# Optimization experiments

Measured on AMD Instinct MI355X. Metric: run time of the kernel, lower is better.

The kernel has to match this reference:

```python
import jax, jax.numpy as jnp
import numpy as np

E = 8        # num_experts
K = 2        # top_k
CAP = 512    # hard-coded capacity in MoELayer
H = 2048     # hidden_dim
F = 8192     # ffn_dim


def setup_inputs() -> dict:
    key = jax.random.key(0)
    ks = jax.random.split(key, 6)
    inp = {
        "hidden_states": jax.random.normal(ks[0], (2, 1024, H), jnp.float32),
        "router_w": jax.random.normal(ks[1], (E, H), jnp.float32) * (0.01 / np.sqrt(H)),
        "w1": jax.random.normal(ks[2], (F, H), jnp.float32) * (1.0 / np.sqrt(H)),
        "b1": jax.random.normal(ks[3], (F,), jnp.float32) * 0.01,
        "w2": jax.random.normal(ks[4], (H, F), jnp.float32) * (1.0 / np.sqrt(F)),
        "b2": jax.random.normal(ks[5], (H,), jnp.float32) * 0.01,
    }
    return inp


def reference(hidden_states, router_w, w1, b1, w2, b2):
    orig_shape = hidden_states.shape
    x = hidden_states.reshape(-1, H)          # [N, H]
    N = x.shape[0]

    # --- Router: softmax then top-k ---
    logits = x @ router_w.T                   # [N, E]
    probs = jax.nn.softmax(logits, axis=-1)
    top_p, top_i = jax.lax.top_k(probs, K)    # [N, K]

    # --- Capacity-based permute (slot-major order: all slot-0 tokens, then slot-1,
    # matching the torch loop over top_k slots within each expert) ---
    expert_flat = top_i.T.reshape(-1)         # [K*N] int
    probs_flat = top_p.T.reshape(-1)          # [K*N]
    token_idx = jnp.tile(jnp.arange(N), K)    # [K*N]

    onehot = (expert_flat[:, None] == jnp.arange(E)[None, :]).astype(jnp.int32)  # [K*N, E]
    # position of each routed token within its expert's queue
    pos = jnp.take_along_axis(jnp.cumsum(onehot, axis=0), expert_flat[:, None], axis=1)[:, 0] - 1
    keep = pos < CAP                          # deterministic truncation at capacity
    dest = expert_flat * CAP + pos            # slot in [E*CAP] dispatch buffer
    dest_m = jnp.where(keep, dest, E * CAP)   # out-of-range -> dropped by scatter

    buf = jnp.zeros((E * CAP, H), x.dtype).at[dest_m].set(x[token_idx], mode='drop')

    # --- Shared expert FFN (all2all is identity on one device) ---
    h = jax.nn.gelu(buf @ w1.T + b1, approximate=False) @ w2.T + b2  # [E*CAP, H]

    # --- Weighted combine (scatter-add back to token positions) ---
    gathered = jnp.where(keep[:, None], h[jnp.where(keep, dest, 0)], 0.0) * probs_flat[:, None]
    out = jnp.zeros_like(x).at[token_idx].add(gathered)
    return out.reshape(orig_shape)
```

## Files before the change

### kernel.cpp

```cpp
#include <hip/hip_runtime.h>

#define HD 2048
#define FD 8192
#define NE 8
#define CAP 512

typedef __attribute__((ext_vector_type(4))) float f32x4;
typedef __attribute__((ext_vector_type(8))) __bf16 bf16x8;

__device__ __forceinline__ void gload_lds16(const __bf16* g, __bf16* l) {
    __builtin_amdgcn_global_load_lds(
        (const __attribute__((address_space(1))) void*)g,
        (__attribute__((address_space(3))) void*)l, 16, 0, 0);
}
__device__ __forceinline__ void waitv4() { asm volatile("s_waitcnt vmcnt(4)" ::: "memory"); }
__device__ __forceinline__ void waitv0() { asm volatile("s_waitcnt vmcnt(0)" ::: "memory"); }

__global__ __launch_bounds__(256) void cvt_k(const float* __restrict__ src,
                                             __bf16* __restrict__ dst, int n8) {
    int i = blockIdx.x * 256 + threadIdx.x;
    if (i >= n8) return;
    const float* s = src + (size_t)i * 8;
    f32x4 a = *(const f32x4*)s;
    f32x4 b = *(const f32x4*)(s + 4);
    bf16x8 o;
    o[0] = (__bf16)a[0]; o[1] = (__bf16)a[1]; o[2] = (__bf16)a[2]; o[3] = (__bf16)a[3];
    o[4] = (__bf16)b[0]; o[5] = (__bf16)b[1]; o[6] = (__bf16)b[2]; o[7] = (__bf16)b[3];
    *(bf16x8*)(dst + (size_t)i * 8) = o;
}

__global__ __launch_bounds__(256) void router_k(const float* __restrict__ x,
                                                const float* __restrict__ rw,
                                                int2* __restrict__ experts,
                                                float2* __restrict__ probs, int Ntok) {
    int wave = threadIdx.x >> 6, lane = threadIdx.x & 63;
    int n = blockIdx.x * 4 + wave;
    if (n >= Ntok) return;
    const float* xr = x + (size_t)n * HD;
    double acc[NE];
#pragma unroll
    for (int e = 0; e < NE; e++) acc[e] = 0.0;
    for (int i = 0; i < HD / 64; i++) {
        float xv = xr[lane + 64 * i];
#pragma unroll
        for (int e = 0; e < NE; e++)
            acc[e] += (double)xv * (double)rw[e * HD + lane + 64 * i];
    }
#pragma unroll
    for (int e = 0; e < NE; e++) {
        double v = acc[e];
        for (int off = 32; off > 0; off >>= 1) v += __shfl_xor(v, off);
        acc[e] = v;
    }
    if (lane == 0) {
        double mx = acc[0];
#pragma unroll
        for (int e = 1; e < NE; e++) mx = acc[e] > mx ? acc[e] : mx;
        double s = 0.0;
#pragma unroll
        for (int e = 0; e < NE; e++) s += exp(acc[e] - mx);
        float pf[NE];
#pragma unroll
        for (int e = 0; e < NE; e++) pf[e] = (float)(exp(acc[e] - mx) / s);
        int e0 = 0; float b0 = pf[0];
#pragma unroll
        for (int e = 1; e < NE; e++) if (pf[e] > b0) { b0 = pf[e]; e0 = e; }
        int e1 = -1; float b1 = -1.0f;
#pragma unroll
        for (int e = 0; e < NE; e++) if (e != e0 && pf[e] > b1) { b1 = pf[e]; e1 = e; }
        experts[n] = make_int2(e0, e1);
        probs[n] = make_float2(b0, b1);
    }
}

__global__ __launch_bounds__(256) void scan_k(const int2* __restrict__ experts,
                                              int* __restrict__ dest,
                                              int* __restrict__ slot_token, int Ntok) {
    __shared__ int cnts[256][NE];
    int tid = threadIdx.x;
    for (int i = tid; i < NE * CAP; i += 256) slot_token[i] = -1;
    int per = (2 * Ntok) / 256;
    int base = tid * per;
    int c[NE];
#pragma unroll
    for (int e = 0; e < NE; e++) c[e] = 0;
    int eloc[16];
    for (int i = 0; i < per; i++) {
        int j = base + i;
        int t = j & (Ntok - 1);
        int2 ex = experts[t];
        int e = (j >= Ntok) ? ex.y : ex.x;
        eloc[i] = e;
        c[e]++;
    }
#pragma unroll
    for (int e = 0; e < NE; e++) cnts[tid][e] = c[e];
    __syncthreads();
    if (tid < NE) {
        int run = 0;
        for (int t2 = 0; t2 < 256; t2++) { int v = cnts[t2][tid]; cnts[t2][tid] = run; run += v; }
    }
    __syncthreads();
    int b[NE];
#pragma unroll
    for (int e = 0; e < NE; e++) b[e] = cnts[tid][e];
    for (int i = 0; i < per; i++) {
        int j = base + i;
        int t = j & (Ntok - 1);
        int e = eloc[i];
        int pos = b[e]++;
        if (pos < CAP) {
            int d = e * CAP + pos;
            dest[j] = d;
            slot_token[d] = t;
        } else {
            dest[j] = -1;
        }
    }
}

__global__ __launch_bounds__(256) void dispatch_k(const float* __restrict__ x,
                                                  const int* __restrict__ slot_token,
                                                  __bf16* __restrict__ buf) {
    int slot = blockIdx.x;
    int tok = slot_token[slot];
    int idx = threadIdx.x * 8;
    __bf16* drow = buf + (size_t)slot * HD + idx;
    if (tok >= 0) {
        const float* srow = x + (size_t)tok * HD + idx;
        f32x4 a = *(const f32x4*)srow;
        f32x4 b = *(const f32x4*)(srow + 4);
        bf16x8 o;
        o[0] = (__bf16)a[0]; o[1] = (__bf16)a[1]; o[2] = (__bf16)a[2]; o[3] = (__bf16)a[3];
        o[4] = (__bf16)b[0]; o[5] = (__bf16)b[1]; o[6] = (__bf16)b[2]; o[7] = (__bf16)b[3];
        *(bf16x8*)drow = o;
    } else {
        f32x4 z = 0;
        *(f32x4*)drow = z;
    }
}

__device__ inline float gelu_exact(float v) {
    return 0.5f * v * (1.0f + erff(v * 0.70710678118654752f));
}

template <int EPI, int BM, int ALOADS, int QM>
__global__ __launch_bounds__(512) void gemm8p(const __bf16* __restrict__ A,
                                              const __bf16* __restrict__ B,
                                              const float* __restrict__ bias,
                                              void* __restrict__ Cout,
                                              int N, int K) {
    constexpr int MREP = 4 * QM;
    __shared__ __align__(16) __bf16 As[2][BM * 64];
    __shared__ __align__(16) __bf16 Bs[2][256 * 64];
    int m0 = blockIdx.y * BM, n0 = blockIdx.x * 256;
    int tid = threadIdx.x;
    int lane = tid & 63, wave = tid >> 6;
    int wr = wave >> 2, wc = wave & 3;
    int lrow = lane & 15, l16 = lane >> 4;
    int NT = K >> 6;

    int sr = tid >> 3;
    int c8 = tid & 7;
    int csw = (c8 ^ (sr & 7)) * 8;
    const __bf16* Ag = A + (size_t)(m0 + sr) * K + csw;
    const __bf16* Bg = B + (size_t)(n0 + sr) * K + csw;
    int ldst = sr * 64 + c8 * 8;

    int rch0 = ((0 + l16) ^ (lrow & 7)) * 8;
    int rch1 = ((4 + l16) ^ (lrow & 7)) * 8;

    f32x4 acc[MREP][4];
#pragma unroll
    for (int m = 0; m < MREP; m++)
#pragma unroll
        for (int n = 0; n < 4; n++) acc[m][n] = 0;

#pragma unroll
    for (int i = 0; i < ALOADS; i++)
        gload_lds16(Ag + (size_t)(i * 64) * K, &As[0][ldst + i * 4096]);
#pragma unroll
    for (int i = 0; i < 4; i++)
        gload_lds16(Bg + (size_t)(i * 64) * K, &Bs[0][ldst + i * 4096]);
#pragma unroll
    for (int i = 0; i < 4; i++)
        gload_lds16(Bg + (size_t)(i * 64) * K + 64, &Bs[1][ldst + i * 4096]);
    waitv4();
    __builtin_amdgcn_s_barrier();

    for (int t = 0; t < NT; ++t) {
        int p = t & 1;
        const __bf16* Asl = As[p];
        const __bf16* Bsl = Bs[p];
        bf16x8 bf[4][2];
#pragma unroll
        for (int q = 0; q < 4; ++q) {
            bf16x8 af[QM][2];
#pragma unroll
            for (int j = 0; j < QM; j++) {
                int row = (wr * (BM / 2) + (q * QM + j) * 16 + lrow) * 64;
                af[j][0] = *(const bf16x8*)&Asl[row + rch0];
                af[j][1] = *(const bf16x8*)&Asl[row + rch1];
            }
            if (q == 0) {
#pragma unroll
                for (int n = 0; n < 4; n++) {
                    int row = (wc * 64 + n * 16 + lrow) * 64;
                    bf[n][0] = *(const bf16x8*)&Bsl[row + rch0];
                    bf[n][1] = *(const bf16x8*)&Bsl[row + rch1];
                }
                if (t + 1 < NT) {
                    gload_lds16(Ag + (size_t)(t + 1) * 64, &As[(t + 1) & 1][ldst]);
                    gload_lds16(Ag + (size_t)64 * K + (size_t)(t + 1) * 64,
                                &As[(t + 1) & 1][ldst + 4096]);
                }
            } else if (q == 1) {
                if (ALOADS == 4 && t + 1 < NT) {
                    gload_lds16(Ag + (size_t)128 * K + (size_t)(t + 1) * 64,
                                &As[(t + 1) & 1][ldst + 8192]);
                    gload_lds16(Ag + (size_t)192 * K + (size_t)(t + 1) * 64,
                                &As[(t + 1) & 1][ldst + 12288]);
                }
            } else if (q == 2) {
                if (t + 2 < NT) {
                    gload_lds16(Bg + (size_t)(t + 2) * 64, &Bs[t & 1][ldst]);
                    gload_lds16(Bg + (size_t)64 * K + (size_t)(t + 2) * 64,
                                &Bs[t & 1][ldst + 4096]);
                }
            } else {
                if (t + 2 < NT) {
                    gload_lds16(Bg + (size_t)128 * K + (size_t)(t + 2) * 64,
                                &Bs[t & 1][ldst + 8192]);
                    gload_lds16(Bg + (size_t)192 * K + (size_t)(t + 2) * 64,
                                &Bs[t & 1][ldst + 12288]);
                }
            }
            __builtin_amdgcn_s_barrier();
            __builtin_amdgcn_s_setprio(1);
#pragma unroll
            for (int j = 0; j < QM; j++)
#pragma unroll
                for (int n = 0; n < 4; n++)
#pragma unroll
                    for (int kk = 0; kk < 2; kk++)
                        acc[q * QM + j][n] = __builtin_amdgcn_mfma_f32_16x16x32_bf16(
                            af[j][kk], bf[n][kk], acc[q * QM + j][n], 0, 0, 0);
            __builtin_amdgcn_s_setprio(0);
            if (q == 3) {
                if (t + 2 < NT) waitv4(); else waitv0();
            }
            __builtin_amdgcn_s_barrier();
        }
    }

    int col_base = n0 + wc * 64;
    int row_base0 = m0 + wr * (BM / 2) + l16 * 4;
#pragma unroll
    for (int n = 0; n < 4; n++) {
        int col = col_base + n * 16 + lrow;
        float bv = bias[col];
#pragma unroll
        for (int mf = 0; mf < MREP; mf++) {
            int row0 = row_base0 + mf * 16;
#pragma unroll
            for (int r = 0; r < 4; r++) {
                float v = acc[mf][n][r] + bv;
                if (EPI == 0) {
                    ((__bf16*)Cout)[(size_t)(row0 + r) * N + col] = (__bf16)gelu_exact(v);
                } else {
                    ((float*)Cout)[(size_t)(row0 + r) * N + col] = v;
                }
            }
        }
    }
}

__global__ __launch_bounds__(256) void combine_k(const float* __restrict__ h2,
                                                 const int* __restrict__ dest,
                                                 const float2* __restrict__ probs,
                                                 float* __restrict__ out, int Ntok) {
    int t = blockIdx.x;
    int d0 = dest[t], d1 = dest[Ntok + t];
    float2 p = probs[t];
    int idx = threadIdx.x * 8;
    f32x4 o0 = 0, o1 = 0;
    if (d0 >= 0) {
        const float* r = h2 + (size_t)d0 * HD + idx;
        o0 += p.x * (*(const f32x4*)r);
        o1 += p.x * (*(const f32x4*)(r + 4));
    }
    if (d1 >= 0) {
        const float* r = h2 + (size_t)d1 * HD + idx;
        o0 += p.y * (*(const f32x4*)r);
        o1 += p.y * (*(const f32x4*)(r + 4));
    }
    float* w = out + (size_t)t * HD + idx;
    *(f32x4*)w = o0;
    *(f32x4*)(w + 4) = o1;
}

extern "C" void kernel_launch(void* const* d_in, const int* in_sizes, int n_in,
                              void* d_out, int out_size, void* d_ws, size_t ws_size,
                              hipStream_t stream) {
    const float* x  = (const float*)d_in[0];
    const float* rw = (const float*)d_in[1];
    const float* w1 = (const float*)d_in[2];
    const float* b1 = (const float*)d_in[3];
    const float* w2 = (const float*)d_in[4];
    const float* b2 = (const float*)d_in[5];
    float* out = (float*)d_out;
    int Ntok = in_sizes[0] / HD;

    char* ws = (char*)d_ws;
    __bf16* w1b = (__bf16*)ws;            ws += (size_t)FD * HD * 2;
    __bf16* w2b = (__bf16*)ws;            ws += (size_t)HD * FD * 2;
    __bf16* buf = (__bf16*)ws;            ws += (size_t)NE * CAP * HD * 2;
    __bf16* h1  = (__bf16*)ws;            ws += (size_t)NE * CAP * FD * 2;
    float*  h2  = (float*)ws;             ws += (size_t)NE * CAP * HD * 4;
    int2*   experts = (int2*)ws;          ws += (size_t)Ntok * 8;
    float2* probsb  = (float2*)ws;        ws += (size_t)Ntok * 8;
    int*    dest    = (int*)ws;           ws += (size_t)2 * Ntok * 4;
    int*    slot_token = (int*)ws;        ws += (size_t)NE * CAP * 4;

    int n8 = FD * HD / 8;
    cvt_k<<<n8 / 256, 256, 0, stream>>>(w1, w1b, n8);
    cvt_k<<<n8 / 256, 256, 0, stream>>>(w2, w2b, n8);
    router_k<<<Ntok / 4, 256, 0, stream>>>(x, rw, experts, probsb, Ntok);
    scan_k<<<1, 256, 0, stream>>>(experts, dest, slot_token, Ntok);
    dispatch_k<<<NE * CAP, 256, 0, stream>>>(x, slot_token, buf);
    gemm8p<0, 256, 4, 2><<<dim3(FD / 256, (NE * CAP) / 256), 512, 0, stream>>>(
        buf, w1b, b1, (void*)h1, FD, HD);
    gemm8p<1, 128, 2, 1><<<dim3(HD / 256, (NE * CAP) / 128), 512, 0, stream>>>(
        h1, w2b, b2, (void*)h2, HD, FD);
    combine_k<<<Ntok, 256, 0, stream>>>(h2, dest, probsb, out, Ntok);
}
```

Baseline: 526.7 us.

## Software-pipeline A-fragment LDS reads across MFMA phases in gemm8p

Restructures the GEMM inner loop so each phase works on two 16-row A fragments. The next phase's A fragment is double-buffered in registers and loaded from LDS before the current phase's MFMAs, with a sched_barrier keeping the order. For the BM=128 GEMM this also changes the phase split from 4 phases of 1 fragment to 2 phases of 2, and regroups the B prefetch loads. The aim is to hide LDS read latency behind MFMA work and cut per-phase barrier overhead, at the cost of more VGPRs for the extra fragment buffers.

After: 563.9 us. 7.1% more time.

```diff
diff --git a/kernel.cpp b/kernel.cpp
--- a/kernel.cpp
+++ b/kernel.cpp
@@ -144,13 +144,15 @@
     return 0.5f * v * (1.0f + erff(v * 0.70710678118654752f));
 }
 
-template <int EPI, int BM, int ALOADS, int QM>
+template <int EPI, int BM>
 __global__ __launch_bounds__(512) void gemm8p(const __bf16* __restrict__ A,
                                               const __bf16* __restrict__ B,
                                               const float* __restrict__ bias,
                                               void* __restrict__ Cout,
                                               int N, int K) {
-    constexpr int MREP = 4 * QM;
+    constexpr int MREP = BM / 32;
+    constexpr int P = MREP / 2;
+    constexpr int ALOADS = BM / 64;
     __shared__ __align__(16) __bf16 As[2][BM * 64];
     __shared__ __align__(16) __bf16 Bs[2][256 * 64];
     int m0 = blockIdx.y * BM, n0 = blockIdx.x * 256;
@@ -189,64 +191,72 @@
     __builtin_amdgcn_s_barrier();
 
     for (int t = 0; t < NT; ++t) {
-        int p = t & 1;
-        const __bf16* Asl = As[p];
-        const __bf16* Bsl = Bs[p];
+        const __bf16* Asl = As[t & 1];
+        const __bf16* Bsl = Bs[t & 1];
+        __bf16* Anx = As[(t + 1) & 1];
+        __bf16* Bnx = Bs[t & 1];
         bf16x8 bf[4][2];
-#pragma unroll
-        for (int q = 0; q < 4; ++q) {
-            bf16x8 af[QM][2];
-#pragma unroll
-            for (int j = 0; j < QM; j++) {
-                int row = (wr * (BM / 2) + (q * QM + j) * 16 + lrow) * 64;
-                af[j][0] = *(const bf16x8*)&Asl[row + rch0];
-                af[j][1] = *(const bf16x8*)&Asl[row + rch1];
-            }
-            if (q == 0) {
-#pragma unroll
-                for (int n = 0; n < 4; n++) {
-                    int row = (wc * 64 + n * 16 + lrow) * 64;
-                    bf[n][0] = *(const bf16x8*)&Bsl[row + rch0];
-                    bf[n][1] = *(const bf16x8*)&Bsl[row + rch1];
-                }
-                if (t + 1 < NT) {
-                    gload_lds16(Ag + (size_t)(t + 1) * 64, &As[(t + 1) & 1][ldst]);
-                    gload_lds16(Ag + (size_t)64 * K + (size_t)(t + 1) * 64,
-                                &As[(t + 1) & 1][ldst + 4096]);
-                }
-            } else if (q == 1) {
-                if (ALOADS == 4 && t + 1 < NT) {
-                    gload_lds16(Ag + (size_t)128 * K + (size_t)(t + 1) * 64,
-                                &As[(t + 1) & 1][ldst + 8192]);
-                    gload_lds16(Ag + (size_t)192 * K + (size_t)(t + 1) * 64,
-                                &As[(t + 1) & 1][ldst + 12288]);
-                }
-            } else if (q == 2) {
-                if (t + 2 < NT) {
-                    gload_lds16(Bg + (size_t)(t + 2) * 64, &Bs[t & 1][ldst]);
-                    gload_lds16(Bg + (size_t)64 * K + (size_t)(t + 2) * 64,
-                                &Bs[t & 1][ldst + 4096]);
+        bf16x8 af[2][2][2];
+#pragma unroll
+        for (int n = 0; n < 4; n++) {
+            int row = (wc * 64 + n * 16 + lrow) * 64;
+            bf[n][0] = *(const bf16x8*)&Bsl[row + rch0];
+            bf[n][1] = *(const bf16x8*)&Bsl[row + rch1];
+        }
+#pragma unroll
+        for (int j = 0; j < 2; j++) {
+            int row = (wr * (BM / 2) + j * 16 + lrow) * 64;
+            af[0][j][0] = *(const bf16x8*)&Asl[row + rch0];
+            af[0][j][1] = *(const bf16x8*)&Asl[row + rch1];
+        }
+#pragma unroll
+        for (int q = 0; q < P; ++q) {
+            if (P == 4) {
+                if (q == 0 && t + 1 < NT) {
+                    gload_lds16(Ag + (size_t)(t + 1) * 64, Anx + ldst);
+                    gload_lds16(Ag + (size_t)64 * K + (size_t)(t + 1) * 64, Anx + ldst + 4096);
+                } else if (q == 1 && t + 1 < NT) {
+                    gload_lds16(Ag + (size_t)128 * K + (size_t)(t + 1) * 64, Anx + ldst + 8192);
+                    gload_lds16(Ag + (size_t)192 * K + (size_t)(t + 1) * 64, Anx + ldst + 12288);
+                } else if (q == 2 && t + 2 < NT) {
+                    gload_lds16(Bg + (size_t)(t + 2) * 64, Bnx + ldst);
+                    gload_lds16(Bg + (size_t)64 * K + (size_t)(t + 2) * 64, Bnx + ldst + 4096);
+                } else if (q == 3 && t + 2 < NT) {
+                    gload_lds16(Bg + (size_t)128 * K + (size_t)(t + 2) * 64, Bnx + ldst + 8192);
+                    gload_lds16(Bg + (size_t)192 * K + (size_t)(t + 2) * 64, Bnx + ldst + 12288);
                 }
             } else {
-                if (t + 2 < NT) {
-                    gload_lds16(Bg + (size_t)128 * K + (size_t)(t + 2) * 64,
-                                &Bs[t & 1][ldst + 8192]);
-                    gload_lds16(Bg + (size_t)192 * K + (size_t)(t + 2) * 64,
-                                &Bs[t & 1][ldst + 12288]);
+                if (q == 0 && t + 1 < NT) {
+                    gload_lds16(Ag + (size_t)(t + 1) * 64, Anx + ldst);
+                    gload_lds16(Ag + (size_t)64 * K + (size_t)(t + 1) * 64, Anx + ldst + 4096);
+                } else if (q == 1 && t + 2 < NT) {
+                    gload_lds16(Bg + (size_t)(t + 2) * 64, Bnx + ldst);
+                    gload_lds16(Bg + (size_t)64 * K + (size_t)(t + 2) * 64, Bnx + ldst + 4096);
+                    gload_lds16(Bg + (size_t)128 * K + (size_t)(t + 2) * 64, Bnx + ldst + 8192);
+                    gload_lds16(Bg + (size_t)192 * K + (size_t)(t + 2) * 64, Bnx + ldst + 12288);
                 }
             }
             __builtin_amdgcn_s_barrier();
+            if (q < P - 1) {
+#pragma unroll
+                for (int j = 0; j < 2; j++) {
+                    int row = (wr * (BM / 2) + ((q + 1) * 2 + j) * 16 + lrow) * 64;
+                    af[(q + 1) & 1][j][0] = *(const bf16x8*)&Asl[row + rch0];
+                    af[(q + 1) & 1][j][1] = *(const bf16x8*)&Asl[row + rch1];
+                }
+            }
+            __builtin_amdgcn_sched_barrier(0);
             __builtin_amdgcn_s_setprio(1);
 #pragma unroll
-            for (int j = 0; j < QM; j++)
+            for (int j = 0; j < 2; j++)
 #pragma unroll
                 for (int n = 0; n < 4; n++)
 #pragma unroll
                     for (int kk = 0; kk < 2; kk++)
-                        acc[q * QM + j][n] = __builtin_amdgcn_mfma_f32_16x16x32_bf16(
-                            af[j][kk], bf[n][kk], acc[q * QM + j][n], 0, 0, 0);
+                        acc[q * 2 + j][n] = __builtin_amdgcn_mfma_f32_16x16x32_bf16(
+                            af[q & 1][j][kk], bf[n][kk], acc[q * 2 + j][n], 0, 0, 0);
             __builtin_amdgcn_s_setprio(0);
-            if (q == 3) {
+            if (q == P - 1) {
                 if (t + 2 < NT) waitv4(); else waitv0();
             }
             __builtin_amdgcn_s_barrier();
@@ -328,9 +338,9 @@
     router_k<<<Ntok / 4, 256, 0, stream>>>(x, rw, experts, probsb, Ntok);
     scan_k<<<1, 256, 0, stream>>>(experts, dest, slot_token, Ntok);
     dispatch_k<<<NE * CAP, 256, 0, stream>>>(x, slot_token, buf);
-    gemm8p<0, 256, 4, 2><<<dim3(FD / 256, (NE * CAP) / 256), 512, 0, stream>>>(
+    gemm8p<0, 256><<<dim3(FD / 256, (NE * CAP) / 256), 512, 0, stream>>>(
         buf, w1b, b1, (void*)h1, FD, HD);
-    gemm8p<1, 128, 2, 1><<<dim3(HD / 256, (NE * CAP) / 128), 512, 0, stream>>>(
+    gemm8p<1, 128><<<dim3(HD / 256, (NE * CAP) / 128), 512, 0, stream>>>(
         h1, w2b, b2, (void*)h2, HD, FD);
     combine_k<<<Ntok, 256, 0, stream>>>(h2, dest, probsb, out, Ntok);
 }
```
